# Kernel optimization log

Measured on AMD Instinct MI355X. Metric: run time of the kernel, lower is better.

Reference implementation:

```python
import jax, jax.numpy as jnp
import numpy as np

M_NUMS = 4096
D_NUMS = 4096
PROJ = 256
EPS = 1e-10


def _lin(x, W, b):
    # torch nn.Linear: y = x @ W.T + b
    return x @ W.T + b


def setup_inputs() -> dict:
    key = jax.random.key(0)
    ks = jax.random.split(key, 16)
    N = M_NUMS + D_NUMS
    inp = {}
    inp["m_d_feat"] = jax.random.normal(ks[0], (N, PROJ), dtype=jnp.float32)
    inp["bigraph"] = jax.random.uniform(ks[1], (N, N), dtype=jnp.float32)
    # sparse-ish binary co-occurrence matrices (values !=0 / ==0 drive masks)
    inp["m_co"] = (jax.random.uniform(ks[2], (M_NUMS, M_NUMS)) < 0.1).astype(jnp.float32)
    inp["d_co"] = (jax.random.uniform(ks[3], (D_NUMS, D_NUMS)) < 0.1).astype(jnp.float32)
    # positive degrees in [1, 50) to keep 1/sqrt and 1/deg well-conditioned
    inp["m_co_deg"] = jax.random.uniform(ks[4], (M_NUMS, 2)) * 49.0 + 1.0
    inp["d_co_deg"] = jax.random.uniform(ks[5], (D_NUMS, 2)) * 49.0 + 1.0
    inp["m_d_degree"] = jax.random.uniform(ks[6], (M_NUMS,)) * 49.0 + 1.0
    inp["d_m_degree"] = jax.random.uniform(ks[7], (D_NUMS,)) * 49.0 + 1.0
    s = 0.02
    inp["Wm"] = jax.random.normal(ks[8], (3, PROJ, PROJ), dtype=jnp.float32) * s
    inp["bm"] = jnp.zeros((3, PROJ), dtype=jnp.float32)
    inp["Wd"] = jax.random.normal(ks[9], (3, PROJ, PROJ), dtype=jnp.float32) * s
    inp["bd"] = jnp.zeros((3, PROJ), dtype=jnp.float32)
    inp["Wx"] = jax.random.normal(ks[10], (8, PROJ, PROJ), dtype=jnp.float32) * s
    inp["bx"] = jnp.zeros((8, PROJ), dtype=jnp.float32)
    inp["central_m"] = jax.random.randint(ks[11], (M_NUMS,), 0, 2, dtype=jnp.int32)
    inp["central_d"] = jax.random.randint(ks[12], (D_NUMS,), 0, 2, dtype=jnp.int32)
    inp["m_nums"] = M_NUMS
    return inp


def _homog_block(feat, co, deg, W, b):
    # self-loop + degree-normalized co-occurrence / non-co-occurrence GEMMs
    n = feat.shape[0]
    diag = jnp.eye(n, dtype=bool)
    co_mask = (~diag) & (co != 0)
    non_mask = (~diag) & (co == 0)
    out = _lin(feat, W[0], b[0])  # self loop
    d0 = deg[:, 0]
    coeff0 = (1.0 / jnp.sqrt(d0[:, None] * d0[None, :] + EPS)) * co_mask.astype(feat.dtype)
    out = out + coeff0 @ _lin(feat, W[1], b[1])
    d1 = deg[:, 1]
    coeff1 = (1.0 / jnp.sqrt(d1[:, None] * d1[None, :] + EPS)) * non_mask.astype(feat.dtype)
    out = out + coeff1 @ _lin(feat, W[2], b[2])
    return out


def _cross_block(assoc, row_central, col_central, norm_row, src_feat, Wx, bx, pairs):
    # sum of 4 (central/normal x central/normal) masked-association GEMMs
    rc = row_central != 0
    cc = col_central != 0
    masks = [
        rc[:, None] & cc[None, :],
        rc[:, None] & (~cc)[None, :],
        (~rc)[:, None] & cc[None, :],
        (~rc)[:, None] & (~cc)[None, :],
    ]
    norm = (1.0 / norm_row)[:, None]
    out = jnp.zeros((assoc.shape[0], src_feat.shape[1]), dtype=src_feat.dtype)
    for mask, (i, j) in zip(masks, pairs):
        transformed = _lin(src_feat, Wx[i], bx[i]) + _lin(src_feat, Wx[j], bx[j])
        out = out + 0.5 * norm * ((assoc * mask.astype(assoc.dtype)) @ transformed)
    return out


def reference(m_d_feat, bigraph, m_co, m_co_deg, d_co, d_co_deg, m_d_degree,
              d_m_degree, Wm, bm, Wd, bd, Wx, bx, central_m, central_d, m_nums):
    m = m_nums
    m_feat = m_d_feat[:m]
    d_feat = m_d_feat[m:]

    out_m = _homog_block(m_feat, m_co, m_co_deg, Wm, bm)
    out_d = _homog_block(d_feat, d_co, d_co_deg, Wd, bd)

    # m <- d aggregation: Wx indices 0..7 =
    # [cm2cd, cd2cm, cm2nd, cd2nm, nm2cd, nd2cm, nm2nd, nd2nm]
    assoc_md = bigraph[:m, m:]
    out_m = out_m + _cross_block(assoc_md, central_m, central_d, m_d_degree,
                                 d_feat, Wx, bx,
                                 pairs=[(0, 1), (2, 5), (4, 3), (6, 7)])
    # d <- m aggregation (roles swapped)
    assoc_dm = bigraph[m:, :m]
    out_d = out_d + _cross_block(assoc_dm, central_d, central_m, d_m_degree,
                                 m_feat, Wx, bx,
                                 pairs=[(1, 0), (3, 4), (5, 2), (7, 6)])

    return jnp.concatenate([out_m, out_d], axis=0)
```

## Files before the change

kernel.cpp:

```cpp
#include <hip/hip_runtime.h>
#include <hip/hip_bf16.h>


typedef __bf16 bf16x8 __attribute__((ext_vector_type(8)));
typedef float floatx4 __attribute__((ext_vector_type(4)));
typedef float f32x4 __attribute__((ext_vector_type(4)));
using bf16 = __hip_bfloat16;

#define LDK 72

__device__ __forceinline__ float b2f(bf16 x){ return __bfloat162float(x); }
__device__ __forceinline__ bf16 f2b(float f){ return __float2bfloat16(f); }
__device__ __forceinline__ float rawb2f(unsigned short u){
  unsigned int x = ((unsigned int)u) << 16; float f; __builtin_memcpy(&f,&x,4); return f;
}
__device__ __forceinline__ unsigned short f2bu(float f){
  bf16 h = __float2bfloat16(f); unsigned short u; __builtin_memcpy(&u,&h,2); return u;
}
__device__ __forceinline__ uint4 cvt8(float4 a, float4 b){
  unsigned short u[8] = {f2bu(a.x),f2bu(a.y),f2bu(a.z),f2bu(a.w),
                         f2bu(b.x),f2bu(b.y),f2bu(b.z),f2bu(b.w)};
  uint4 v; __builtin_memcpy(&v,u,16); return v;
}
__device__ __forceinline__ void async_ld16(const void* gp, void* lp){
  typedef __attribute__((address_space(1))) const unsigned int GU;
  typedef __attribute__((address_space(3))) unsigned int LU;
  __builtin_amdgcn_global_load_lds((GU*)(unsigned long long)gp,
                                   (LU*)(unsigned int)(unsigned long long)lp,
                                   16, 0, 0);
}

__global__ void prep_kernel(const float* __restrict__ m_co_deg, const float* __restrict__ d_co_deg,
                            const float* __restrict__ m_d_degree, const float* __restrict__ d_m_degree,
                            const float* __restrict__ Wx, const float* __restrict__ bx,
                            float* __restrict__ scal, float* __restrict__ Sbuf, float* __restrict__ bSbuf)
{
  const int i = blockIdx.x*blockDim.x + threadIdx.x;
  if (i < 4096){
    scal[0*4096+i] = rsqrtf(m_co_deg[2*i]);
    scal[1*4096+i] = rsqrtf(m_co_deg[2*i+1]);
    scal[2*4096+i] = 0.5f / m_d_degree[i];
    scal[3*4096+i] = rsqrtf(d_co_deg[2*i]);
    scal[4*4096+i] = rsqrtf(d_co_deg[2*i+1]);
    scal[5*4096+i] = 0.5f / d_m_degree[i];
  }
  const int pa[4] = {0,2,3,6}, pb[4] = {1,5,4,7};
  if (i < 65536){
    #pragma unroll
    for (int s=0;s<4;s++)
      Sbuf[s*65536+i] = Wx[pa[s]*65536+i] + Wx[pb[s]*65536+i];
  }
  if (i < 256){
    #pragma unroll
    for (int s=0;s<4;s++)
      bSbuf[s*256+i] = bx[pa[s]*256+i] + bx[pb[s]*256+i];
  }
}

__global__ __launch_bounds__(256) void stage1_kernel(
    const float* __restrict__ feat, const float* __restrict__ Wm, const float* __restrict__ bm,
    const float* __restrict__ Wd, const float* __restrict__ bd,
    const float* __restrict__ Sbuf, const float* __restrict__ bSbuf, const float* __restrict__ scal,
    bf16* __restrict__ BHm, bf16* __restrict__ BHd,
    float* __restrict__ L0m, float* __restrict__ L0d,
    float* __restrict__ L2nm, float* __restrict__ L2nd,
    bf16* __restrict__ Tm, bf16* __restrict__ Td)
{
  __shared__ __align__(16) bf16 As[128*LDK];
  __shared__ __align__(16) bf16 Bs[128*LDK];
  const int p = blockIdx.y;
  const int side = p >> 3, widx = p & 7;
  const int bx_ = blockIdx.x;
  const bool modeT = (widx != 0 && widx != 7);
  const float* X = feat + (size_t)side*(4096*256);
  const float* Wb = side ? Wd : Wm;
  const float* W = (widx==0) ? Wb : (widx==7) ? (Wb + 2*65536)
                 : (widx<=2) ? (Wb + widx*65536) : (Sbuf + (widx-3)*65536);
  int rt, ct;
  if (!modeT){ rt = bx_>>1; ct = bx_&1; } else { rt = bx_&1; ct = bx_>>1; }
  const float* Amat = modeT ? W : X;
  const float* Bmat = modeT ? X : W;
  const int arow0 = rt*128, brow0 = ct*128;
  const int tid = threadIdx.x;
  const int lane = tid & 63, wv = tid>>6;
  const int wr = wv>>1, wc = wv&1, q = lane>>4, l15 = lane&15;

  floatx4 acc[4][4];
  #pragma unroll
  for (int i=0;i<4;i++)
    #pragma unroll
    for (int j=0;j<4;j++)
      #pragma unroll
      for (int r=0;r<4;r++) acc[i][j][r] = 0.f;

  for (int kt=0; kt<4; kt++){
    const int c0 = kt*64;
    __syncthreads();
    #pragma unroll
    for (int i=0;i<4;i++){
      const int id = tid + i*256;
      const int row = id>>3, kg = id&7;
      const float* ap = Amat + (size_t)(arow0+row)*256 + c0 + kg*8;
      const float* bp = Bmat + (size_t)(brow0+row)*256 + c0 + kg*8;
      float4 a0 = *(const float4*)ap, a1 = *(const float4*)(ap+4);
      float4 b0 = *(const float4*)bp, b1 = *(const float4*)(bp+4);
      *(uint4*)(&As[row*LDK + kg*8]) = cvt8(a0,a1);
      *(uint4*)(&Bs[row*LDK + kg*8]) = cvt8(b0,b1);
    }
    __syncthreads();
    #pragma unroll
    for (int ki=0; ki<2; ki++){
      bf16x8 af[4], bg[4];
      #pragma unroll
      for (int i=0;i<4;i++) af[i] = *(const bf16x8*)&As[(wr*64 + i*16 + l15)*LDK + ki*32 + q*8];
      #pragma unroll
      for (int j=0;j<4;j++) bg[j] = *(const bf16x8*)&Bs[(wc*64 + j*16 + l15)*LDK + ki*32 + q*8];
      #pragma unroll
      for (int i=0;i<4;i++)
        #pragma unroll
        for (int j=0;j<4;j++)
          acc[i][j] = __builtin_amdgcn_mfma_f32_16x16x32_bf16(af[i], bg[j], acc[i][j], 0,0,0);
    }
  }

  const float* bb = side ? bd : bm;
  const float* bias = (widx==0) ? bb : (widx==7) ? (bb + 512)
                    : (widx<=2) ? (bb + widx*256) : (bSbuf + (widx-3)*256);
  float* outF = nullptr; bf16* outB = nullptr; int pitch = 256; const float* scl = nullptr;
  if (widx==0){ outF = side? L0d : L0m; }
  else if (widx==7){ outF = side? L2nd : L2nm; }
  else if (widx==1){ outB = side? BHd : BHm; pitch = 4096; scl = scal + side*12288; }
  else if (widx==2){ outB = (side? BHd : BHm) + 256*4096; pitch = 4096; scl = scal + side*12288 + 4096; }
  else { outB = (side? Td : Tm) + (widx-3)*(256*4096); pitch = 4096; }

  #pragma unroll
  for (int i=0;i<4;i++){
    #pragma unroll
    for (int j=0;j<4;j++){
      const int gcol = brow0 + wc*64 + j*16 + l15;
      #pragma unroll
      for (int r=0;r<4;r++){
        const int grow = arow0 + wr*64 + i*16 + q*4 + r;
        float v = acc[i][j][r];
        const int nidx = modeT ? grow : gcol;
        v += bias[nidx];
        if (scl) v *= scl[gcol];
        if (outF) outF[(size_t)grow*pitch + gcol] = v;
        else      outB[(size_t)grow*pitch + gcol] = f2b(v);
      }
    }
  }
}

__global__ void stage2_kernel(const bf16* __restrict__ Tm, const bf16* __restrict__ Td,
                              const int* __restrict__ central_m, const int* __restrict__ central_d,
                              bf16* __restrict__ BXm, bf16* __restrict__ BXd)
{
  const int idx = blockIdx.x*blockDim.x + threadIdx.x;
  const int oside = idx >> 20;
  const int rem = idx & 1048575;
  const int n = rem >> 12;
  const int c = rem & 4095;
  const bf16* T = oside ? Tm : Td;
  const int* cen = oside ? central_m : central_d;
  bf16* B = oside ? BXd : BXm;
  const bool cc = cen[c] != 0;
  int v0i, v1i;
  if (!oside){ v0i = cc ? 2 : 3; v1i = cc ? 0 : 1; }
  else       { v0i = cc ? 1 : 3; v1i = cc ? 0 : 2; }
  const float v0 = b2f(T[(size_t)v0i*1048576 + (size_t)n*4096 + c]);
  const float v1 = b2f(T[(size_t)v1i*1048576 + (size_t)n*4096 + c]);
  B[(size_t)n*4096 + c]         = f2b(v0);
  B[(size_t)(256+n)*4096 + c]   = f2b(v1 - v0);
}

__global__ void colsum_kernel(const bf16* __restrict__ BHm, const bf16* __restrict__ BHd,
                              float* __restrict__ Scol)
{
  const int b = blockIdx.x;
  const int sd = b >> 8, n = b & 255;
  const int lane = threadIdx.x;
  const bf16* rowp = (sd ? BHd : BHm) + (size_t)(256+n)*4096;
  float s = 0.f;
  #pragma unroll
  for (int t=0;t<8;t++){
    const uint4 v = *(const uint4*)(rowp + t*512 + lane*8);
    unsigned short u[8]; __builtin_memcpy(u,&v,16);
    #pragma unroll
    for (int jj=0;jj<8;jj++) s += rawb2f(u[jj]);
  }
  #pragma unroll
  for (int off=32; off>0; off>>=1) s += __shfl_down(s, off);
  if (lane==0) Scol[sd*256 + n] = s;
}

__global__ __launch_bounds__(512,2) void gemm_kernel(
    const float* __restrict__ bigraph, const float* __restrict__ m_co, const float* __restrict__ d_co,
    const int* __restrict__ central_m, const int* __restrict__ central_d,
    const float* __restrict__ scal,
    const bf16* __restrict__ BHm, const bf16* __restrict__ BHd,
    const bf16* __restrict__ BXm, const bf16* __restrict__ BXd,
    float* __restrict__ partial)
{
  __shared__ __align__(16) bf16 As[2][128*32];
  __shared__ __align__(16) bf16 Bs[3][512*32];
  const int bid = blockIdx.x;
  const int w = (bid & 7)*32 + (bid >> 3);
  const int seg = w & 1, mt = (w >> 1) & 31, p = w >> 6;
  const int s = p & 1;
  const bool maskmode = (p < 2);
  const int k0 = seg*2048;
  const int rowbase = mt*128;
  const float* Asrc; int apitch; int acoff;
  if (p==0){ Asrc = m_co; apitch = 4096; acoff = 0; }
  else if (p==1){ Asrc = d_co; apitch = 4096; acoff = 0; }
  else if (p==2){ Asrc = bigraph; apitch = 8192; acoff = 4096; }
  else { Asrc = bigraph + (size_t)4096*8192; apitch = 8192; acoff = 0; }
  const bf16* B0 = (p==0) ? BHm : (p==1) ? BHd : (p==2) ? BXm : BXd;

  const int tid = threadIdx.x;
  const int lane = tid&63, wv = tid>>6;
  const int wr = wv>>2, wc = wv&3;
  const int q = lane>>4, l15 = lane&15;

  const int a_row = tid>>2, a_sg = tid&3;
  const int a_g  = a_sg ^ ((a_row>>1)&3);
  const int a_gr = rowbase + a_row;
  const float* a_base = Asrc + (size_t)a_gr*apitch + acoff + a_g*8;
  int b_roff[4]; int b_ldsoff[4];
  #pragma unroll
  for (int j=0;j<4;j++){
    const int cb = wv*256 + j*64;
    const int chunk = cb + lane;
    const int row = chunk>>2, sg = chunk&3;
    const int gg = sg ^ ((row>>1)&3);
    b_roff[j] = row*4096 + gg*8;
    b_ldsoff[j] = cb*8;
  }
  int af_off[4], bf_off[4];
  #pragma unroll
  for (int i=0;i<4;i++){
    const int ra = wr*64 + i*16 + l15;
    af_off[i] = ra*32 + ((q ^ ((ra>>1)&3)))*8;
  }
  #pragma unroll
  for (int j=0;j<4;j++){
    const int rb = wc*64 + j*16 + l15;
    bf_off[j] = rb*32 + ((q ^ ((rb>>1)&3)))*8;
  }

  floatx4 acc0[4][4], acc1[4][4];
  #pragma unroll
  for (int i=0;i<4;i++)
    #pragma unroll
    for (int j=0;j<4;j++)
      #pragma unroll
      for (int r=0;r<4;r++){ acc0[i][j][r] = 0.f; acc1[i][j][r] = 0.f; }

  auto issueB = [&](int kkg, int buf){
    #pragma unroll
    for (int j=0;j<4;j++)
      async_ld16(B0 + (size_t)b_roff[j] + kkg, &Bs[buf][b_ldsoff[j]]);
  };
  auto writeA = [&](f32x4 a0, f32x4 a1, int kkg, int buf){
    const float av[8] = {a0[0],a0[1],a0[2],a0[3],a1[0],a1[1],a1[2],a1[3]};
    unsigned short u[8];
    if (maskmode){
      const int cbase = kkg + a_g*8;
      #pragma unroll
      for (int jj=0;jj<8;jj++)
        u[jj] = (av[jj]!=0.0f && (cbase+jj)!=a_gr) ? (unsigned short)0x3F80 : (unsigned short)0;
    } else {
      #pragma unroll
      for (int jj=0;jj<8;jj++) u[jj] = f2bu(av[jj]);
    }
    uint4 w4; __builtin_memcpy(&w4,u,16);
    *(uint4*)(&As[buf][tid*8]) = w4;
  };

  {
    const float* ap = a_base + k0;
    f32x4 a0 = __builtin_nontemporal_load((const f32x4*)ap);
    f32x4 a1 = __builtin_nontemporal_load((const f32x4*)(ap+4));
    __builtin_amdgcn_sched_barrier(0);
    issueB(k0, 0);
    issueB(k0 + 32, 1);
    __builtin_amdgcn_sched_barrier(0);
    writeA(a0, a1, k0, 0);
    asm volatile("s_waitcnt vmcnt(4) lgkmcnt(0)" ::: "memory");
    __builtin_amdgcn_s_barrier();
    __builtin_amdgcn_sched_barrier(0);
  }

  int bcur = 0;
  for (int kt=0; kt<64; kt++){
    const int curA = kt & 1;
    const bool pre1 = (kt+1 < 64);
    const bool pre2 = (kt+2 < 64);
    f32x4 a0, a1;
    if (pre1){
      const float* ap = a_base + k0 + (kt+1)*32;
      a0 = __builtin_nontemporal_load((const f32x4*)ap);
      a1 = __builtin_nontemporal_load((const f32x4*)(ap+4));
    }
    __builtin_amdgcn_sched_barrier(0);
    if (pre2){
      const int bw = (bcur+2 < 3) ? bcur+2 : bcur-1;
      issueB(k0 + (kt+2)*32, bw);
    }
    __builtin_amdgcn_sched_barrier(0);
    {
      const bf16* AsC = &As[curA][0];
      const bf16* BsC = &Bs[bcur][0];
      bf16x8 af[4];
      #pragma unroll
      for (int i=0;i<4;i++) af[i] = *(const bf16x8*)&AsC[af_off[i]];
      #pragma unroll
      for (int j=0;j<4;j++){
        const bf16x8 b0 = *(const bf16x8*)&BsC[bf_off[j]];
        const bf16x8 b1 = *(const bf16x8*)&BsC[256*32 + bf_off[j]];
        #pragma unroll
        for (int i=0;i<4;i++){
          acc0[i][j] = __builtin_amdgcn_mfma_f32_16x16x32_bf16(af[i], b0, acc0[i][j], 0,0,0);
          acc1[i][j] = __builtin_amdgcn_mfma_f32_16x16x32_bf16(af[i], b1, acc1[i][j], 0,0,0);
        }
      }
    }
    __builtin_amdgcn_sched_barrier(0);
    if (pre1) writeA(a0, a1, k0 + (kt+1)*32, curA^1);
    asm volatile("s_waitcnt lgkmcnt(0)" ::: "memory");
    __builtin_amdgcn_s_barrier();
    __builtin_amdgcn_sched_barrier(0);
    bcur = (bcur+1 < 3) ? bcur+1 : 0;
  }

  const float* scS = scal + (size_t)s*12288;
  const int* cenR = s ? central_d : central_m;
  float* pb = partial + ((size_t)seg*4 + p)*4096*256;
  #pragma unroll
  for (int i=0;i<4;i++){
    #pragma unroll
    for (int r_=0;r_<4;r_++){
      const int rl = rowbase + wr*64 + i*16 + q*4 + r_;
      float w0, w1;
      if (maskmode){ w0 = scS[rl]; w1 = -scS[4096+rl]; }
      else { const float nr = scS[8192+rl]; w0 = nr; w1 = cenR[rl] ? nr : 0.f; }
      #pragma unroll
      for (int j=0;j<4;j++){
        const int gcol = wc*64 + j*16 + l15;
        pb[(size_t)rl*256 + gcol] = w0*acc0[i][j][r_] + w1*acc1[i][j][r_];
      }
    }
  }
}

__global__ void reduce_kernel(const float* __restrict__ partial,
                              const float* __restrict__ L0m, const float* __restrict__ L0d,
                              const float* __restrict__ L2nm, const float* __restrict__ L2nd,
                              const float* __restrict__ Scol, const float* __restrict__ scal,
                              float* __restrict__ out)
{
  const int idx = blockIdx.x*blockDim.x + threadIdx.x;
  const int r = idx >> 6;
  const int n4 = (idx & 63) << 2;
  const int s = r >> 12;
  const int rl = r & 4095;
  const float r1 = scal[s*12288 + 4096 + rl];
  const size_t rb = (size_t)rl*256 + n4;
  const float4 l0 = *(const float4*)((s? L0d : L0m) + rb);
  const float4 l2 = *(const float4*)((s? L2nd : L2nm) + rb);
  const float4 sc = *(const float4*)(Scol + s*256 + n4);
  const float4 h0 = *(const float4*)(partial + (size_t)(0*4+s)*1048576 + rb);
  const float4 h1 = *(const float4*)(partial + (size_t)(1*4+s)*1048576 + rb);
  const float4 x0 = *(const float4*)(partial + (size_t)(0*4+2+s)*1048576 + rb);
  const float4 x1 = *(const float4*)(partial + (size_t)(1*4+2+s)*1048576 + rb);
  const float r1sq = r1*r1;
  float4 o;
  o.x = l0.x + h0.x+h1.x + x0.x+x1.x + r1*sc.x - r1sq*l2.x;
  o.y = l0.y + h0.y+h1.y + x0.y+x1.y + r1*sc.y - r1sq*l2.y;
  o.z = l0.z + h0.z+h1.z + x0.z+x1.z + r1*sc.z - r1sq*l2.z;
  o.w = l0.w + h0.w+h1.w + x0.w+x1.w + r1*sc.w - r1sq*l2.w;
  *(float4*)(out + (size_t)r*256 + n4) = o;
}

extern "C" void kernel_launch(void* const* d_in, const int* in_sizes, int n_in,
                              void* d_out, int out_size, void* d_ws, size_t ws_size,
                              hipStream_t stream)
{
  (void)in_sizes; (void)n_in; (void)out_size; (void)ws_size;
  const float* m_d_feat   = (const float*)d_in[0];
  const float* bigraph    = (const float*)d_in[1];
  const float* m_co       = (const float*)d_in[2];
  const float* d_co       = (const float*)d_in[3];
  const float* m_co_deg   = (const float*)d_in[4];
  const float* d_co_deg   = (const float*)d_in[5];
  const float* m_d_degree = (const float*)d_in[6];
  const float* d_m_degree = (const float*)d_in[7];
  const float* Wm = (const float*)d_in[8];
  const float* bm = (const float*)d_in[9];
  const float* Wd = (const float*)d_in[10];
  const float* bd = (const float*)d_in[11];
  const float* Wx = (const float*)d_in[12];
  const float* bx = (const float*)d_in[13];
  const int* central_m = (const int*)d_in[14];
  const int* central_d = (const int*)d_in[15];

  char* ws = (char*)d_ws;
  bf16*  BHm  = (bf16*) (ws + 0);
  bf16*  BHd  = (bf16*) (ws + 4194304);
  bf16*  BXm  = (bf16*) (ws + 8388608);
  bf16*  BXd  = (bf16*) (ws + 12582912);
  float* L0m  = (float*)(ws + 16777216);
  float* L0d  = (float*)(ws + 20971520);
  float* L2nm = (float*)(ws + 25165824);
  float* L2nd = (float*)(ws + 29360128);
  float* Sbuf = (float*)(ws + 33554432);
  float* bSbuf= (float*)(ws + 34603008);
  float* scal = (float*)(ws + 34607104);
  float* Scol = (float*)(ws + 34705408);
  bf16*  Tm   = (bf16*) (ws + 34707456);
  bf16*  Td   = (bf16*) (ws + 43096064);
  float* partial = (float*)(ws + 34707456);

  prep_kernel<<<256, 256, 0, stream>>>(m_co_deg, d_co_deg, m_d_degree, d_m_degree,
                                       Wx, bx, scal, Sbuf, bSbuf);
  stage1_kernel<<<dim3(64,16), 256, 0, stream>>>(m_d_feat, Wm, bm, Wd, bd, Sbuf, bSbuf, scal,
                                                 BHm, BHd, L0m, L0d, L2nm, L2nd, Tm, Td);
  stage2_kernel<<<8192, 256, 0, stream>>>(Tm, Td, central_m, central_d, BXm, BXd);
  colsum_kernel<<<512, 64, 0, stream>>>(BHm, BHd, Scol);
  gemm_kernel<<<256, 512, 0, stream>>>(bigraph, m_co, d_co, central_m, central_d,
                                       scal, BHm, BHd, BXm, BXd, partial);
  reduce_kernel<<<2048, 256, 0, stream>>>(partial, L0m, L0d, L2nm, L2nd, Scol, scal, (float*)d_out);
}
```

Baseline: 548.8 us.

## Deepen A-operand prefetch to two tiles and raise wave priority around MFMAs

The main GEMM loop is unrolled by two with separate even and odd register sets for the fp32 A tile, so A global loads are issued two k-steps ahead instead of one. The loads now have a full extra iteration to land before they are converted and written to LDS. All B fragments are loaded from LDS before the MFMA block, which is wrapped in s_setprio to favour the matrix instructions. This raises VGPR pressure (extra A registers plus eight B fragments), which may lower occupancy.

After: 568.0 us. 3.5% more time.

```diff
diff --git a/kernel.cpp b/kernel.cpp
--- a/kernel.cpp
+++ b/kernel.cpp
@@ -277,61 +277,94 @@
     uint4 w4; __builtin_memcpy(&w4,u,16);
     *(uint4*)(&As[buf][tid*8]) = w4;
   };
+  auto computeOn = [&](const bf16* AsC, const bf16* BsC){
+    bf16x8 af[4];
+    #pragma unroll
+    for (int i=0;i<4;i++) af[i] = *(const bf16x8*)&AsC[af_off[i]];
+    bf16x8 b0v[4], b1v[4];
+    #pragma unroll
+    for (int j=0;j<4;j++){
+      b0v[j] = *(const bf16x8*)&BsC[bf_off[j]];
+      b1v[j] = *(const bf16x8*)&BsC[256*32 + bf_off[j]];
+    }
+    __builtin_amdgcn_s_setprio(1);
+    #pragma unroll
+    for (int j=0;j<4;j++)
+      #pragma unroll
+      for (int i=0;i<4;i++){
+        acc0[i][j] = __builtin_amdgcn_mfma_f32_16x16x32_bf16(af[i], b0v[j], acc0[i][j], 0,0,0);
+        acc1[i][j] = __builtin_amdgcn_mfma_f32_16x16x32_bf16(af[i], b1v[j], acc1[i][j], 0,0,0);
+      }
+    __builtin_amdgcn_s_setprio(0);
+  };
+
+  f32x4 a_ev0, a_ev1, a_od0, a_od1;
+  int bcur = 0;
 
   {
-    const float* ap = a_base + k0;
-    f32x4 a0 = __builtin_nontemporal_load((const f32x4*)ap);
-    f32x4 a1 = __builtin_nontemporal_load((const f32x4*)(ap+4));
+    const float* ap0 = a_base + k0;
+    a_ev0 = __builtin_nontemporal_load((const f32x4*)ap0);
+    a_ev1 = __builtin_nontemporal_load((const f32x4*)(ap0+4));
     __builtin_amdgcn_sched_barrier(0);
     issueB(k0, 0);
     issueB(k0 + 32, 1);
     __builtin_amdgcn_sched_barrier(0);
-    writeA(a0, a1, k0, 0);
-    asm volatile("s_waitcnt vmcnt(4) lgkmcnt(0)" ::: "memory");
+    const float* ap1 = a_base + k0 + 32;
+    a_od0 = __builtin_nontemporal_load((const f32x4*)ap1);
+    a_od1 = __builtin_nontemporal_load((const f32x4*)(ap1+4));
+    __builtin_amdgcn_sched_barrier(0);
+    writeA(a_ev0, a_ev1, k0, 0);
+    asm volatile("s_waitcnt vmcnt(6) lgkmcnt(0)" ::: "memory");
     __builtin_amdgcn_s_barrier();
     __builtin_amdgcn_sched_barrier(0);
   }
 
-  int bcur = 0;
-  for (int kt=0; kt<64; kt++){
-    const int curA = kt & 1;
-    const bool pre1 = (kt+1 < 64);
-    const bool pre2 = (kt+2 < 64);
-    f32x4 a0, a1;
-    if (pre1){
-      const float* ap = a_base + k0 + (kt+1)*32;
-      a0 = __builtin_nontemporal_load((const f32x4*)ap);
-      a1 = __builtin_nontemporal_load((const f32x4*)(ap+4));
-    }
-    __builtin_amdgcn_sched_barrier(0);
-    if (pre2){
-      const int bw = (bcur+2 < 3) ? bcur+2 : bcur-1;
-      issueB(k0 + (kt+2)*32, bw);
-    }
-    __builtin_amdgcn_sched_barrier(0);
+  #pragma unroll 1
+  for (int kt = 0; kt < 64; kt += 2){
     {
-      const bf16* AsC = &As[curA][0];
-      const bf16* BsC = &Bs[bcur][0];
-      bf16x8 af[4];
-      #pragma unroll
-      for (int i=0;i<4;i++) af[i] = *(const bf16x8*)&AsC[af_off[i]];
-      #pragma unroll
-      for (int j=0;j<4;j++){
-        const bf16x8 b0 = *(const bf16x8*)&BsC[bf_off[j]];
-        const bf16x8 b1 = *(const bf16x8*)&BsC[256*32 + bf_off[j]];
-        #pragma unroll
-        for (int i=0;i<4;i++){
-          acc0[i][j] = __builtin_amdgcn_mfma_f32_16x16x32_bf16(af[i], b0, acc0[i][j], 0,0,0);
-          acc1[i][j] = __builtin_amdgcn_mfma_f32_16x16x32_bf16(af[i], b1, acc1[i][j], 0,0,0);
-        }
-      }
-    }
-    __builtin_amdgcn_sched_barrier(0);
-    if (pre1) writeA(a0, a1, k0 + (kt+1)*32, curA^1);
-    asm volatile("s_waitcnt lgkmcnt(0)" ::: "memory");
-    __builtin_amdgcn_s_barrier();
-    __builtin_amdgcn_sched_barrier(0);
-    bcur = (bcur+1 < 3) ? bcur+1 : 0;
+      const bool pre2 = (kt+2 < 64);
+      if (pre2){
+        const int bw = (bcur+2 < 3) ? bcur+2 : bcur-1;
+        issueB(k0 + (kt+2)*32, bw);
+      }
+      __builtin_amdgcn_sched_barrier(0);
+      if (pre2){
+        const float* ap = a_base + k0 + (kt+2)*32;
+        a_ev0 = __builtin_nontemporal_load((const f32x4*)ap);
+        a_ev1 = __builtin_nontemporal_load((const f32x4*)(ap+4));
+      }
+      __builtin_amdgcn_sched_barrier(0);
+      computeOn(&As[0][0], &Bs[bcur][0]);
+      __builtin_amdgcn_sched_barrier(0);
+      writeA(a_od0, a_od1, k0 + (kt+1)*32, 1);
+      asm volatile("s_waitcnt lgkmcnt(0)" ::: "memory");
+      __builtin_amdgcn_s_barrier();
+      __builtin_amdgcn_sched_barrier(0);
+      bcur = (bcur+1 < 3) ? bcur+1 : 0;
+    }
+    {
+      const int kt1 = kt + 1;
+      const bool pre2 = (kt1+2 < 64);
+      const bool pre1 = (kt1+1 < 64);
+      if (pre2){
+        const int bw = (bcur+2 < 3) ? bcur+2 : bcur-1;
+        issueB(k0 + (kt1+2)*32, bw);
+      }
+      __builtin_amdgcn_sched_barrier(0);
+      if (pre2){
+        const float* ap = a_base + k0 + (kt1+2)*32;
+        a_od0 = __builtin_nontemporal_load((const f32x4*)ap);
+        a_od1 = __builtin_nontemporal_load((const f32x4*)(ap+4));
+      }
+      __builtin_amdgcn_sched_barrier(0);
+      computeOn(&As[1][0], &Bs[bcur][0]);
+      __builtin_amdgcn_sched_barrier(0);
+      if (pre1) writeA(a_ev0, a_ev1, k0 + (kt1+1)*32, 0);
+      asm volatile("s_waitcnt lgkmcnt(0)" ::: "memory");
+      __builtin_amdgcn_s_barrier();
+      __builtin_amdgcn_sched_barrier(0);
+      bcur = (bcur+1 < 3) ? bcur+1 : 0;
+    }
   }
 
   const float* scS = scal + (size_t)s*12288;
```
